# Kernel optimization log

Measured on AMD Instinct MI355X. Metric: run time of the kernel, lower is better.

Reference implementation:

```python
import jax, jax.numpy as jnp
import numpy as np

B, T, C, H = 2, 2048, 1024, 16
D = C // H
SCALE = 1.0 / np.sqrt(D).astype(np.float32)


def setup_inputs() -> dict:
    key = jax.random.key(0)
    kx, kq, kk, kv, ko = jax.random.split(key, 5)
    s = 1.0 / np.sqrt(C).astype(np.float32)
    return {
        "x": jax.random.normal(kx, (B, T, C), dtype=jnp.float32),
        "wq": jax.random.normal(kq, (C, C), dtype=jnp.float32) * s,
        "wk": jax.random.normal(kk, (C, C), dtype=jnp.float32) * s,
        "wv": jax.random.normal(kv, (C, C), dtype=jnp.float32) * s,
        "wo": jax.random.normal(ko, (C, C), dtype=jnp.float32) * s,
    }


def reference(x, wq, wk, wv, wo):
    # nn.Linear(y) = y @ W.T; weights stored [out, in]
    q = (x @ wq.T).reshape(B, T, H, D).transpose(0, 2, 1, 3)  # [B,H,T,D]
    k = (x @ wk.T).reshape(B, T, H, D).transpose(0, 2, 1, 3)
    v = (x @ wv.T).reshape(B, T, H, D).transpose(0, 2, 1, 3)
    scores = jnp.einsum("bhqd,bhkd->bhqk", q, k) * SCALE  # [B,H,T,T]
    causal = jnp.tril(jnp.ones((T, T), dtype=bool))
    scores = jnp.where(causal, scores, -jnp.inf)
    attn = jax.nn.softmax(scores, axis=-1)
    out = jnp.einsum("bhqk,bhkd->bhqd", attn, v)  # [B,H,T,D]
    out = out.transpose(0, 2, 1, 3).reshape(B, T, C)
    return out @ wo.T
```

## Files before the change

### kernel.cpp

```cpp
#include <hip/hip_runtime.h>
#include <hip/hip_bf16.h>

#define B_ 2
#define T_ 2048
#define C_ 1024
#define H_ 16
#define D_ 64
#define M_ (B_*T_)
#define SCALE_ 0.125f
#define LOG2E_ 1.44269504f
#define NEG_ (-1e30f)
#define MOFF_ 12.0f

typedef __bf16 bf16;
typedef __bf16 bf16x4 __attribute__((ext_vector_type(4)));
typedef __bf16 bf16x8 __attribute__((ext_vector_type(8)));
typedef float  f32x4  __attribute__((ext_vector_type(4)));

#define XB_ELEMS  ((size_t)M_*C_)
#define W_ELEMS   ((size_t)C_*C_)

__device__ __forceinline__ void glds16(const void* g, void* l) {
  __builtin_amdgcn_global_load_lds((const __attribute__((address_space(1))) void*)g,
                                   (__attribute__((address_space(3))) void*)l,
                                   16, 0, 0);
}

__global__ __launch_bounds__(256)
void cvt5(const float* __restrict__ x,  const float* __restrict__ wq,
          const float* __restrict__ wk, const float* __restrict__ wv,
          const float* __restrict__ wo, bf16* __restrict__ out,
          bf16* __restrict__ wodst) {
  int bid = blockIdx.x;
  const float* src; bf16* dst; size_t off;
  if (bid < 2048)      { src = x;  dst = out;                         off = (size_t)bid*2048; }
  else if (bid < 2560) { src = wq; dst = out + XB_ELEMS;              off = (size_t)(bid-2048)*2048; }
  else if (bid < 3072) { src = wk; dst = out + XB_ELEMS +   W_ELEMS;  off = (size_t)(bid-2560)*2048; }
  else if (bid < 3584) { src = wv; dst = out + XB_ELEMS + 2*W_ELEMS;  off = (size_t)(bid-3072)*2048; }
  else                 { src = wo; dst = wodst;                       off = (size_t)(bid-3584)*2048; }
  size_t i = off + (size_t)threadIdx.x * 8;
  f32x4 lo = *(const f32x4*)(src + i);
  f32x4 hi = *(const f32x4*)(src + i + 4);
  bf16x8 r;
  #pragma unroll
  for (int t = 0; t < 4; ++t) { r[t] = (bf16)lo[t]; r[t+4] = (bf16)hi[t]; }
  *(bf16x8*)(dst + i) = r;
}

template<int OUTMODE>
__global__ __launch_bounds__(256)
void gemm_nt(const bf16* __restrict__ Ab,
             const bf16* __restrict__ W0, const bf16* __restrict__ W1,
             const bf16* __restrict__ W2,
             void* __restrict__ O0v, void* __restrict__ O1v, void* __restrict__ O2v,
             int K) {
  __shared__ __align__(16) bf16 As[128*64];
  __shared__ __align__(16) bf16 Bs[128*64];

  const bf16* W = W0;
  void* Ov = O0v;
  bool vtrans = false;
  float oscale = 1.0f;
  if constexpr (OUTMODE == 0) {
    if (blockIdx.z == 0)      { oscale = SCALE_ * LOG2E_; }
    else if (blockIdx.z == 1) { W = W1; Ov = O1v; }
    else                      { W = W2; Ov = O2v; vtrans = true; }
  }

  const int m0 = blockIdx.y * 128, n0 = blockIdx.x * 128;
  const int tid = threadIdx.x, wid = tid >> 6, lane = tid & 63;
  const int wm = wid >> 1, wn = wid & 1;
  const int l15 = lane & 15, grp = lane >> 4;

  f32x4 acc[4][4] = {};

  const int lr8 = lane >> 3;
  const int lkswz = ((lane & 7) ^ lr8) * 8;
  const bf16* Ag = Ab + (size_t)(m0 + wid*8 + lr8) * K + lkswz;
  const bf16* Bg = W  + (size_t)(n0 + wid*8 + lr8) * K + lkswz;

  const int amRow = wm*64 + l15;
  const int bnRow = wn*64 + l15;
  const int swz = l15 & 7;

  for (int k0 = 0; k0 < K; k0 += 64) {
    __syncthreads();
    #pragma unroll
    for (int c = 0; c < 4; ++c) {
      glds16(Ag + (size_t)(c*32)*K + k0, As + (wid + c*4)*512);
      glds16(Bg + (size_t)(c*32)*K + k0, Bs + (wid + c*4)*512);
    }
    __syncthreads();

    #pragma unroll
    for (int ks = 0; ks < 2; ++ks) {
      const int aslot = ((ks*4 + grp) ^ swz) * 8;
      bf16x8 af[4], bfr[4];
      #pragma unroll
      for (int i = 0; i < 4; ++i) {
        af[i]  = *(const bf16x8*)(As + (amRow + i*16)*64 + aslot);
        bfr[i] = *(const bf16x8*)(Bs + (bnRow + i*16)*64 + aslot);
      }
      __builtin_amdgcn_s_setprio(1);
      #pragma unroll
      for (int i = 0; i < 4; ++i)
        #pragma unroll
        for (int j = 0; j < 4; ++j)
          acc[i][j] = __builtin_amdgcn_mfma_f32_16x16x32_bf16(af[i], bfr[j], acc[i][j], 0, 0, 0);
      __builtin_amdgcn_s_setprio(0);
    }
  }

  const int rBase = m0 + wm*64 + grp * 4;
  const int cBase = n0 + wn*64 + l15;
  if constexpr (OUTMODE == 0) {
    if (vtrans) {
      #pragma unroll
      for (int fm = 0; fm < 4; ++fm) {
        #pragma unroll
        for (int fn = 0; fn < 4; ++fn) {
          int m = rBase + fm*16;
          int n = cBase + fn*16;
          int b = m >> 11, t = m & 2047, h = n >> 6, d = n & 63;
          bf16x4 pk;
          #pragma unroll
          for (int j = 0; j < 4; ++j) pk[j] = (bf16)(acc[fm][fn][j]);
          *(bf16x4*)((bf16*)Ov + ((size_t)(b*H_ + h) * D_ + d) * T_ + t) = pk;
        }
      }
    } else {
      #pragma unroll
      for (int fm = 0; fm < 4; ++fm) {
        #pragma unroll
        for (int fn = 0; fn < 4; ++fn) {
          #pragma unroll
          for (int j = 0; j < 4; ++j) {
            int m = rBase + fm*16 + j;
            int n = cBase + fn*16;
            int b = m >> 11, t = m & 2047, h = n >> 6, d = n & 63;
            ((bf16*)Ov)[((size_t)(b*H_ + h) * T_ + t) * D_ + d] =
                (bf16)(acc[fm][fn][j] * oscale);
          }
        }
      }
    }
  } else {
    #pragma unroll
    for (int fm = 0; fm < 4; ++fm) {
      #pragma unroll
      for (int fn = 0; fn < 4; ++fn) {
        #pragma unroll
        for (int j = 0; j < 4; ++j) {
          int m = rBase + fm*16 + j;
          int n = cBase + fn*16;
          ((float*)Ov)[(size_t)m * C_ + n] = acc[fm][fn][j];
        }
      }
    }
  }
}

__global__ __launch_bounds__(512)
void attn_fwd(const bf16* __restrict__ Q, const bf16* __restrict__ Km,
              const bf16* __restrict__ Vt, bf16* __restrict__ Oa) {
  __shared__ __align__(16) bf16 Kd[2][64*64];
  __shared__ __align__(16) bf16 Vd[2][64*64];
  __shared__ __align__(16) bf16 Ps[2][64*64];

  const int id = blockIdx.x;
  const int qt = (id < 256) ? (15 - (id >> 5)) : ((id - 256) >> 5);
  const int bh = id & 31;
  const int tid = threadIdx.x, wid = tid >> 6, lane = tid & 63;
  const int ss = wid >> 2;
  const int w4 = wid & 3;
  const int l15 = lane & 15;
  const int grp = lane >> 4;
  const int myrow4 = grp * 4;
  const int sw = l15 & 7;

  const int q0 = qt*128 + ss*64;
  const int ktmax = 2*qt + 1;
  const int diag  = 2*qt + ss;

  const bf16* Qb = Q  + (size_t)bh * T_ * D_;
  const bf16* Kb = Km + (size_t)bh * T_ * D_;
  const bf16* Vb = Vt + (size_t)bh * D_ * T_;

  const int ksr = tid >> 3, kskc = tid & 7;
  const int wsl = (kskc ^ (ksr & 7)) * 8;
  const int b = bh >> 4, h = bh & 15;

  const int qrow = q0 + w4*16 + l15;
  bf16x8 aq0 = *(const bf16x8*)(Qb + (size_t)qrow*64 +      grp*8);
  bf16x8 aq1 = *(const bf16x8*)(Qb + (size_t)qrow*64 + 32 + grp*8);

  f32x4 oacc[4] = {};
  float l_s = 0.f;

  bf16x8 kv_a = *(const bf16x8*)(Kb + (size_t)ksr*64 + kskc*8);
  bf16x8 vt_a = *(const bf16x8*)(Vb + (size_t)ksr*T_ + kskc*8);
  *(bf16x8*)(Kd[0] + ksr*64 + wsl) = kv_a;
  *(bf16x8*)(Vd[0] + ksr*64 + wsl) = vt_a;
  {
    const int kn = (ktmax > 0) ? 64 : 0;
    kv_a = *(const bf16x8*)(Kb + (size_t)(kn + ksr)*64 + kskc*8);
    vt_a = *(const bf16x8*)(Vb + (size_t)ksr*T_ + kn + kskc*8);
  }
  __syncthreads();

  const int prow = w4*16 + l15;
  bf16* Pss = Ps[ss];

  for (int kt = 0; kt <= ktmax; ++kt) {
    const int kv0 = kt * 64;
    const int cur = kt & 1;
    const bf16* Kc = Kd[cur];
    const bf16* Vc = Vd[cur];

    if (kt <= diag) {
      f32x4 s[4];
      __builtin_amdgcn_s_setprio(1);
      #pragma unroll
      for (int n = 0; n < 4; ++n) {
        int row = n*16 + l15;
        bf16x8 bk0 = *(const bf16x8*)(Kc + row*64 + ((grp     ^ sw)*8));
        bf16x8 bk1 = *(const bf16x8*)(Kc + row*64 + (((grp|4) ^ sw)*8));
        f32x4 a = {};
        a = __builtin_amdgcn_mfma_f32_16x16x32_bf16(bk0, aq0, a, 0, 0, 0);
        a = __builtin_amdgcn_mfma_f32_16x16x32_bf16(bk1, aq1, a, 0, 0, 0);
        s[n] = a;
      }
      __builtin_amdgcn_s_setprio(0);

      bf16x8 bv0[4];
      #pragma unroll
      for (int n = 0; n < 4; ++n)
        bv0[n] = *(const bf16x8*)(Vc + (n*16 + l15)*64 + ((grp ^ sw)*8));

      if (kt == diag) {
        #pragma unroll
        for (int n = 0; n < 4; ++n)
          #pragma unroll
          for (int j = 0; j < 4; ++j) {
            int kvg = kv0 + n*16 + myrow4 + j;
            s[n][j] = (kvg <= qrow) ? s[n][j] : NEG_;
          }
      }

      float ps = 0.f;
      #pragma unroll
      for (int n = 0; n < 4; ++n) {
        bf16x4 pw;
        #pragma unroll
        for (int j = 0; j < 4; ++j) {
          float p = __builtin_amdgcn_exp2f(s[n][j] - MOFF_);
          ps += p;
          pw[j] = (bf16)p;
        }
        int sl = (2*n + (grp >> 1)) ^ sw;
        *(bf16x4*)(Pss + prow*64 + sl*8 + (grp & 1)*4) = pw;
      }
      l_s += ps;

      asm volatile("s_waitcnt lgkmcnt(0)" ::: "memory");
      __builtin_amdgcn_sched_barrier(0);

      bf16x8 pa0 = *(const bf16x8*)(Pss + prow*64 + ((grp     ^ sw)*8));
      bf16x8 pa1 = *(const bf16x8*)(Pss + prow*64 + (((grp|4) ^ sw)*8));
      __builtin_amdgcn_s_setprio(1);
      #pragma unroll
      for (int n = 0; n < 4; ++n) {
        bf16x8 bv1 = *(const bf16x8*)(Vc + (n*16 + l15)*64 + (((grp|4) ^ sw)*8));
        oacc[n] = __builtin_amdgcn_mfma_f32_16x16x32_bf16(pa0, bv0[n], oacc[n], 0, 0, 0);
        oacc[n] = __builtin_amdgcn_mfma_f32_16x16x32_bf16(pa1, bv1,    oacc[n], 0, 0, 0);
      }
      __builtin_amdgcn_s_setprio(0);
    }

    if (kt < ktmax) {
      *(bf16x8*)(Kd[cur^1] + ksr*64 + wsl) = kv_a;
      *(bf16x8*)(Vd[cur^1] + ksr*64 + wsl) = vt_a;
      const int kn = (kt + 2 <= ktmax) ? (kv0 + 128) : (kv0 + 64);
      kv_a = *(const bf16x8*)(Kb + (size_t)(kn + ksr)*64 + kskc*8);
      vt_a = *(const bf16x8*)(Vb + (size_t)ksr*T_ + kn + kskc*8);
    }
    __syncthreads();
  }

  l_s += __shfl_xor(l_s, 16);
  l_s += __shfl_xor(l_s, 32);
  const int tg = q0 + w4*16 + myrow4;
  #pragma unroll
  for (int j = 0; j < 4; ++j) {
    float lj = __shfl(l_s, myrow4 + j);
    float inv = 1.f / lj;
    int trow = tg + j;
    #pragma unroll
    for (int n = 0; n < 4; ++n) {
      int ch = h*64 + n*16 + l15;
      Oa[((size_t)(b*T_ + trow)) * C_ + ch] = (bf16)(oacc[n][j] * inv);
    }
  }
}

extern "C" void kernel_launch(void* const* d_in, const int* in_sizes, int n_in,
                              void* d_out, int out_size, void* d_ws, size_t ws_size,
                              hipStream_t stream) {
  const float* x  = (const float*)d_in[0];
  const float* wq = (const float*)d_in[1];
  const float* wk = (const float*)d_in[2];
  const float* wv = (const float*)d_in[3];
  const float* wo = (const float*)d_in[4];

  bf16* q  = (bf16*)d_ws;
  bf16* k  = q  + XB_ELEMS;
  bf16* v  = k  + XB_ELEMS;

  bf16* cvtbuf = (bf16*)d_out;
  bf16* xb  = cvtbuf;
  bf16* wqb = cvtbuf + XB_ELEMS;
  bf16* wkb = wqb + W_ELEMS;
  bf16* wvb = wkb + W_ELEMS;
  bf16* wob_stage = wvb + W_ELEMS;

  const bool bigws = ws_size >= (4*XB_ELEMS + W_ELEMS) * sizeof(bf16);
  bf16* ao  = bigws ? (v + XB_ELEMS) : xb;
  bf16* wob = bigws ? (v + 2*XB_ELEMS) : wob_stage;

  dim3 blk(256);
  cvt5<<<dim3(4096), blk, 0, stream>>>(x, wq, wk, wv, wo, cvtbuf, wob);
  gemm_nt<0><<<dim3(C_/128, M_/128, 3), blk, 0, stream>>>(xb, wqb, wkb, wvb,
                                                          q, k, v, C_);
  attn_fwd<<<dim3(512), dim3(512), 0, stream>>>(q, k, v, ao);
  bf16* aoSrc = ao;
  if (!bigws) {
    hipMemcpyAsync(q, xb,        XB_ELEMS * sizeof(bf16), hipMemcpyDeviceToDevice, stream);
    hipMemcpyAsync(k, wob_stage, W_ELEMS  * sizeof(bf16), hipMemcpyDeviceToDevice, stream);
    aoSrc = q; wob = k;
  }
  gemm_nt<1><<<dim3(C_/128, M_/128, 1), blk, 0, stream>>>(aoSrc, wob, nullptr, nullptr,
                                                          d_out, nullptr, nullptr, C_);
}
```

Baseline: 96.83 us.

## Software-pipeline attention loop: overlap PV of previous tile with QK of current

```diff
diff --git a/kernel.cpp b/kernel.cpp
--- a/kernel.cpp
+++ b/kernel.cpp
@@ -160,12 +160,12 @@
   }
 }
 
-__global__ __launch_bounds__(512)
+__global__ __launch_bounds__(512, 4)
 void attn_fwd(const bf16* __restrict__ Q, const bf16* __restrict__ Km,
               const bf16* __restrict__ Vt, bf16* __restrict__ Oa) {
   __shared__ __align__(16) bf16 Kd[2][64*64];
   __shared__ __align__(16) bf16 Vd[2][64*64];
-  __shared__ __align__(16) bf16 Ps[2][64*64];
+  __shared__ __align__(16) bf16 Ps[2][2][64*64];
 
   const int id = blockIdx.x;
   const int qt = (id < 256) ? (15 - (id >> 5)) : ((id - 256) >> 5);
@@ -196,6 +196,7 @@
 
   f32x4 oacc[4] = {};
   float l_s = 0.f;
+  bf16x8 bvp0[4], bvp1[4];
 
   bf16x8 kv_a = *(const bf16x8*)(Kb + (size_t)ksr*64 + kskc*8);
   bf16x8 vt_a = *(const bf16x8*)(Vb + (size_t)ksr*T_ + kskc*8);
@@ -209,16 +210,18 @@
   __syncthreads();
 
   const int prow = w4*16 + l15;
-  bf16* Pss = Ps[ss];
+  bf16* Pss = Ps[ss][0];
 
   for (int kt = 0; kt <= ktmax; ++kt) {
     const int kv0 = kt * 64;
     const int cur = kt & 1;
     const bf16* Kc = Kd[cur];
     const bf16* Vc = Vd[cur];
-
-    if (kt <= diag) {
-      f32x4 s[4];
+    const bool doQK = (kt <= diag);
+    const bool doPV = (kt >= 1) && (kt <= diag + 1);
+
+    f32x4 s[4];
+    if (doQK) {
       __builtin_amdgcn_s_setprio(1);
       #pragma unroll
       for (int n = 0; n < 4; ++n) {
@@ -231,12 +234,22 @@
         s[n] = a;
       }
       __builtin_amdgcn_s_setprio(0);
-
-      bf16x8 bv0[4];
-      #pragma unroll
-      for (int n = 0; n < 4; ++n)
-        bv0[n] = *(const bf16x8*)(Vc + (n*16 + l15)*64 + ((grp ^ sw)*8));
-
+    }
+
+    if (doPV) {
+      const bf16* Pprev = Pss + (size_t)(cur^1)*4096;
+      bf16x8 pa0 = *(const bf16x8*)(Pprev + prow*64 + ((grp     ^ sw)*8));
+      bf16x8 pa1 = *(const bf16x8*)(Pprev + prow*64 + (((grp|4) ^ sw)*8));
+      __builtin_amdgcn_s_setprio(1);
+      #pragma unroll
+      for (int n = 0; n < 4; ++n) {
+        oacc[n] = __builtin_amdgcn_mfma_f32_16x16x32_bf16(pa0, bvp0[n], oacc[n], 0, 0, 0);
+        oacc[n] = __builtin_amdgcn_mfma_f32_16x16x32_bf16(pa1, bvp1[n], oacc[n], 0, 0, 0);
+      }
+      __builtin_amdgcn_s_setprio(0);
+    }
+
+    if (doQK) {
       if (kt == diag) {
         #pragma unroll
         for (int n = 0; n < 4; ++n)
@@ -248,6 +261,7 @@
       }
 
       float ps = 0.f;
+      bf16* Pw = Pss + (size_t)cur*4096;
       #pragma unroll
       for (int n = 0; n < 4; ++n) {
         bf16x4 pw;
@@ -258,23 +272,15 @@
           pw[j] = (bf16)p;
         }
         int sl = (2*n + (grp >> 1)) ^ sw;
-        *(bf16x4*)(Pss + prow*64 + sl*8 + (grp & 1)*4) = pw;
+        *(bf16x4*)(Pw + prow*64 + sl*8 + (grp & 1)*4) = pw;
       }
       l_s += ps;
 
-      asm volatile("s_waitcnt lgkmcnt(0)" ::: "memory");
-      __builtin_amdgcn_sched_barrier(0);
-
-      bf16x8 pa0 = *(const bf16x8*)(Pss + prow*64 + ((grp     ^ sw)*8));
-      bf16x8 pa1 = *(const bf16x8*)(Pss + prow*64 + (((grp|4) ^ sw)*8));
-      __builtin_amdgcn_s_setprio(1);
       #pragma unroll
       for (int n = 0; n < 4; ++n) {
-        bf16x8 bv1 = *(const bf16x8*)(Vc + (n*16 + l15)*64 + (((grp|4) ^ sw)*8));
-        oacc[n] = __builtin_amdgcn_mfma_f32_16x16x32_bf16(pa0, bv0[n], oacc[n], 0, 0, 0);
-        oacc[n] = __builtin_amdgcn_mfma_f32_16x16x32_bf16(pa1, bv1,    oacc[n], 0, 0, 0);
-      }
-      __builtin_amdgcn_s_setprio(0);
+        bvp0[n] = *(const bf16x8*)(Vc + (n*16 + l15)*64 + ((grp     ^ sw)*8));
+        bvp1[n] = *(const bf16x8*)(Vc + (n*16 + l15)*64 + (((grp|4) ^ sw)*8));
+      }
     }
 
     if (kt < ktmax) {
@@ -285,6 +291,19 @@
       vt_a = *(const bf16x8*)(Vb + (size_t)ksr*T_ + kn + kskc*8);
     }
     __syncthreads();
+  }
+
+  if (diag == ktmax) {
+    asm volatile("s_waitcnt lgkmcnt(0)" ::: "memory");
+    __builtin_amdgcn_sched_barrier(0);
+    const bf16* Plast = Pss + (size_t)(ktmax & 1)*4096;
+    bf16x8 pa0 = *(const bf16x8*)(Plast + prow*64 + ((grp     ^ sw)*8));
+    bf16x8 pa1 = *(const bf16x8*)(Plast + prow*64 + (((grp|4) ^ sw)*8));
+    #pragma unroll
+    for (int n = 0; n < 4; ++n) {
+      oacc[n] = __builtin_amdgcn_mfma_f32_16x16x32_bf16(pa0, bvp0[n], oacc[n], 0, 0, 0);
+      oacc[n] = __builtin_amdgcn_mfma_f32_16x16x32_bf16(pa1, bvp1[n], oacc[n], 0, 0, 0);
+    }
   }
 
   l_s += __shfl_xor(l_s, 16);
```

After: 98.48 us. About the same (+1.7%).
